# Performance work log

Hardware: AMD Instinct MI355X
Metric: run time of the kernel (lower is better)

Reference implementation:

```python
import jax, jax.numpy as jnp
import numpy as np

K = 6  # number of deformation subdivision steps
LEVEL = 5  # icosphere subdivision level -> 10242 verts, 20480 faces
EPS = 1e-12


def _icosphere(level):
    t = (1.0 + 5.0 ** 0.5) / 2.0
    verts = np.array([
        [-1, t, 0], [1, t, 0], [-1, -t, 0], [1, -t, 0],
        [0, -1, t], [0, 1, t], [0, -1, -t], [0, 1, -t],
        [t, 0, -1], [t, 0, 1], [-t, 0, -1], [-t, 0, 1]], dtype=np.float64)
    verts /= np.linalg.norm(verts, axis=1, keepdims=True)
    faces = [[0, 11, 5], [0, 5, 1], [0, 1, 7], [0, 7, 10], [0, 10, 11],
             [1, 5, 9], [5, 11, 4], [11, 10, 2], [10, 7, 6], [7, 1, 8],
             [3, 9, 4], [3, 4, 2], [3, 2, 6], [3, 6, 8], [3, 8, 9],
             [4, 9, 5], [2, 4, 11], [6, 2, 10], [8, 6, 7], [9, 8, 1]]
    for _ in range(level):
        vlist = [v for v in verts]
        cache = {}
        def mid(a, b):
            key = (min(a, b), max(a, b))
            if key not in cache:
                m = vlist[a] + vlist[b]
                m = m / np.linalg.norm(m)
                vlist.append(m)
                cache[key] = len(vlist) - 1
            return cache[key]
        new_faces = []
        for a, b, c in faces:
            ab, bc, ca = mid(a, b), mid(b, c), mid(c, a)
            new_faces += [[a, ab, ca], [b, bc, ab], [c, ca, bc], [ab, bc, ca]]
        faces = new_faces
        verts = np.stack(vlist)
    return verts.astype(np.float32), np.asarray(faces, dtype=np.int32)


def _norm(a):
    return a / jnp.maximum(jnp.linalg.norm(a, axis=-1, keepdims=True), EPS)


def setup_inputs() -> dict:
    key = jax.random.key(0)
    v_np, f_np = _icosphere(LEVEL)  # [10242,3], [20480,3]
    x = jax.random.normal(key, (v_np.shape[0], 6), dtype=jnp.float32)
    return {"x": x, "v": jnp.asarray(v_np), "f": jnp.asarray(f_np)}


def _forward(x, v, f):
    # Build rotation frame from the 6D feature
    rot_x = _norm(x[..., :3])
    rot_z = _norm(jnp.cross(rot_x, x[..., 3:]))
    rot_y = _norm(jnp.cross(rot_z, rot_x))
    # Axis-angle of the rotation matrix with rows (rot_x, rot_y, rot_z)
    axis = jnp.concatenate([
        rot_y[..., 2:3] - rot_z[..., 1:2],
        rot_z[..., 0:1] - rot_x[..., 2:3],
        rot_x[..., 1:2] - rot_y[..., 0:1]], axis=-1)
    trace = (rot_x[..., 0:1] + rot_y[..., 1:2] + rot_z[..., 2:3] - 1.0) * 0.5
    trace = jnp.clip(trace, -1.0 + 1e-7, 1.0 - 1e-7)
    angle = -jnp.arccos(trace) / (2 ** K)
    axis = _norm(axis)
    # Rodrigues rotation of mesh vertices by angle/2^k about per-point axis
    dot = jnp.sum(axis * v, axis=-1, keepdims=True)
    cross = jnp.cross(axis, v)
    cos, sin = jnp.cos(angle), jnp.sin(angle)
    p = v * cos + cross * sin + axis * (dot * (1.0 - cos))  # [N,3]
    # Nearest-triangle search data: face centers on the sphere
    centers = _norm(v[f].mean(axis=1))  # [F,3]
    for _ in range(K):
        p = _norm(p)
        # Nearest face by center direction; [N,F] score matrix (memory-bound)
        fid = jnp.argmax(p @ centers.T, axis=-1)  # [N]
        tri = v[f[fid]]  # [N,3,3] gathered triangle vertices
        # Gnomonic barycentric coords: solve [v0 v1 v2] b = p, normalize
        b = jnp.linalg.solve(jnp.swapaxes(tri, -1, -2), p[..., None])[..., 0]
        bary = b / jnp.sum(b, axis=-1, keepdims=True)  # [N,3]
        # Barycentric gather-interpolate of current point field
        p = jnp.sum(p[f[fid]] * bary[..., None], axis=-2)  # [N,3]
    return _norm(p)


def reference(x, v, f):
    return _forward(x, v, f)
```

## Files before the change

kernel.cpp:

```cpp
#include <hip/hip_runtime.h>
#include <hip/hip_bf16.h>
#include <math.h>

#define EPSN 1e-12f
#define MARGIN 0.02f
#define NBLK 256
#define NTHR 1024

typedef unsigned long long u64;
union F4U { float4 f; u64 u[2]; };

__device__ __forceinline__ float4 cload(const float4* p)
{
    F4U r;
    const u64* q = (const u64*)p;
    r.u[0] = __hip_atomic_load(q + 0, __ATOMIC_RELAXED, __HIP_MEMORY_SCOPE_AGENT);
    r.u[1] = __hip_atomic_load(q + 1, __ATOMIC_RELAXED, __HIP_MEMORY_SCOPE_AGENT);
    return r.f;
}

__device__ __forceinline__ void cstore(float4* p, float4 v)
{
    F4U s; s.f = v;
    u64* q = (u64*)p;
    __hip_atomic_store(q + 0, s.u[0], __ATOMIC_RELAXED, __HIP_MEMORY_SCOPE_AGENT);
    __hip_atomic_store(q + 1, s.u[1], __ATOMIC_RELAXED, __HIP_MEMORY_SCOPE_AGENT);
}

__device__ __forceinline__ int cload_i(const int* p)
{
    return __hip_atomic_load(p, __ATOMIC_RELAXED, __HIP_MEMORY_SCOPE_AGENT);
}

__device__ __forceinline__ void cstore_i(int* p, int v)
{
    __hip_atomic_store(p, v, __ATOMIC_RELAXED, __HIP_MEMORY_SCOPE_AGENT);
}

__global__ __launch_bounds__(1024)
void zero_kernel(int* __restrict__ flags)
{
    for (int i = threadIdx.x; i < 8192; i += 1024) flags[i] = 0;
}

__device__ __forceinline__ void grid_barrier(int* __restrict__ arrive,
                                             int* __restrict__ release,
                                             int target)
{
    asm volatile("s_waitcnt vmcnt(0)" ::: "memory");
    __syncthreads();
    if (threadIdx.x == 0)
        cstore_i(&arrive[blockIdx.x * 16], target);
    if (blockIdx.x == 0 && threadIdx.x < 64) {
        const int l = threadIdx.x;
        for (;;) {
            int a0 = cload_i(&arrive[l * 16]);
            int a1 = cload_i(&arrive[(l + 64) * 16]);
            int a2 = cload_i(&arrive[(l + 128) * 16]);
            int a3 = cload_i(&arrive[(l + 192) * 16]);
            if (__all(min(min(a0, a1), min(a2, a3)) >= target)) break;
            __builtin_amdgcn_s_sleep(2);
        }
        if (l == 0) cstore_i(release, target);
    }
    if (threadIdx.x == 0) {
        while (cload_i(release) < target)
            __builtin_amdgcn_s_sleep(2);
    }
    __syncthreads();
}

__global__ __launch_bounds__(NTHR)
void persist_kernel(const float* __restrict__ x,
                    const float* __restrict__ v,
                    const int* __restrict__ f,
                    float4* __restrict__ fine4,
                    float4* __restrict__ coarse4,
                    float4* __restrict__ v4,
                    float4* __restrict__ pA,
                    float4* __restrict__ pB,
                    float* __restrict__ out,
                    int* __restrict__ arrive,
                    int* __restrict__ release,
                    int N, int F)
{
    const int tid  = threadIdx.x;
    const int lane = tid & 63;
    const int t    = blockIdx.x * NTHR + tid;
    const int gw   = t >> 6;
    const int NW   = (NBLK * NTHR) >> 6;
    const int C    = F >> 6;

    if (gw < C) {
        int fi = (gw << 6) + lane;
        int a = f[fi * 3 + 0], b = f[fi * 3 + 1], c = f[fi * 3 + 2];
        float mx = v[a * 3 + 0] + v[b * 3 + 0] + v[c * 3 + 0];
        float my = v[a * 3 + 1] + v[b * 3 + 1] + v[c * 3 + 1];
        float mz = v[a * 3 + 2] + v[b * 3 + 2] + v[c * 3 + 2];
        float r = 1.0f / fmaxf(sqrtf(mx * mx + my * my + mz * mz), EPSN);
        float fx = mx * r, fy = my * r, fz = mz * r;
        cstore(&fine4[fi], make_float4(fx, fy, fz, 0.0f));
        float sx = fx, sy = fy, sz = fz;
        for (int off = 32; off >= 1; off >>= 1) {
            sx += __shfl_xor(sx, off);
            sy += __shfl_xor(sy, off);
            sz += __shfl_xor(sz, off);
        }
        if (lane == 0) {
            float rr = 1.0f / fmaxf(sqrtf(sx * sx + sy * sy + sz * sz), EPSN);
            cstore(&coarse4[gw], make_float4(sx * rr, sy * rr, sz * rr, 0.0f));
        }
    }

    if (t < N) {
        float ax = x[t * 6 + 0], ay = x[t * 6 + 1], az = x[t * 6 + 2];
        float bx = x[t * 6 + 3], by = x[t * 6 + 4], bz = x[t * 6 + 5];

        float l = fmaxf(sqrtf(ax * ax + ay * ay + az * az), EPSN);
        float rxx = ax / l, rxy = ay / l, rxz = az / l;
        float czx = rxy * bz - rxz * by;
        float czy = rxz * bx - rxx * bz;
        float czz = rxx * by - rxy * bx;
        l = fmaxf(sqrtf(czx * czx + czy * czy + czz * czz), EPSN);
        float rzx = czx / l, rzy = czy / l, rzz = czz / l;
        float cyx = rzy * rxz - rzz * rxy;
        float cyy = rzz * rxx - rzx * rxz;
        float cyz = rzx * rxy - rzy * rxx;
        l = fmaxf(sqrtf(cyx * cyx + cyy * cyy + cyz * cyz), EPSN);
        float ryx = cyx / l, ryy = cyy / l, ryz = cyz / l;

        float axx = ryz - rzy;
        float axy = rzx - rxz;
        float axz = rxy - ryx;
        float trace = (rxx + ryy + rzz - 1.0f) * 0.5f;
        trace = fminf(fmaxf(trace, -1.0f + 1e-7f), 1.0f - 1e-7f);
        float angle = -acosf(trace) * (1.0f / 64.0f);
        l = fmaxf(sqrtf(axx * axx + axy * axy + axz * axz), EPSN);
        axx /= l; axy /= l; axz /= l;

        float vx = v[t * 3 + 0], vy = v[t * 3 + 1], vz = v[t * 3 + 2];
        float d = axx * vx + axy * vy + axz * vz;
        float crx = axy * vz - axz * vy;
        float cry = axz * vx - axx * vz;
        float crz = axx * vy - axy * vx;
        float s, c;
        sincosf(angle, &s, &c);
        float omc = 1.0f - c;
        cstore(&pA[t], make_float4(vx * c + crx * s + axx * (d * omc),
                                   vy * c + cry * s + axy * (d * omc),
                                   vz * c + crz * s + axz * (d * omc), 0.0f));
        cstore(&v4[t], make_float4(vx, vy, vz, 0.0f));
    }

    grid_barrier(arrive, release, 1);

    float4 c0 = coarse4[lane];
    float4 c1 = coarse4[lane + 64];
    float4 c2 = coarse4[lane + 128];
    float4 c3 = coarse4[lane + 192];
    float4 c4 = coarse4[lane + 256];

    const float4* pin = pA;
    float4* pout = pB;

    #pragma unroll 1
    for (int k = 0; k < 6; ++k) {
        const bool last = (k == 5);
        for (int pt = gw; pt < N; pt += NW) {
            float4 p = cload(&pin[pt]);
            float rl = 1.0f / fmaxf(sqrtf(p.x * p.x + p.y * p.y + p.z * p.z), EPSN);
            float pnx = p.x * rl, pny = p.y * rl, pnz = p.z * rl;

            float s0 = pnx * c0.x + pny * c0.y + pnz * c0.z;
            float s1 = pnx * c1.x + pny * c1.y + pnz * c1.z;
            float s2 = pnx * c2.x + pny * c2.y + pnz * c2.z;
            float s3 = pnx * c3.x + pny * c3.y + pnz * c3.z;
            float s4 = pnx * c4.x + pny * c4.y + pnz * c4.z;

            float bs = fmaxf(fmaxf(fmaxf(s0, s1), fmaxf(s2, s3)), s4);
            for (int off = 32; off >= 1; off >>= 1)
                bs = fmaxf(bs, __shfl_xor(bs, off));
            const float thr = bs - MARGIN;

            float best = -1e30f;
            int bidx = 0;
            unsigned long long m;
            #define EXPAND(CC)                                                \
                {                                                             \
                    int cand = ((CC) << 6) + lane;                            \
                    float4 fc = fine4[cand];                                  \
                    float sc = pnx * fc.x + pny * fc.y + pnz * fc.z;          \
                    if (sc > best) { best = sc; bidx = cand; }                \
                }
            m = __ballot(s0 >= thr);
            while (m) { int src = __ffsll(m) - 1; m &= m - 1; EXPAND(src); }
            m = __ballot(s1 >= thr);
            while (m) { int src = __ffsll(m) - 1; m &= m - 1; EXPAND(src + 64); }
            m = __ballot(s2 >= thr);
            while (m) { int src = __ffsll(m) - 1; m &= m - 1; EXPAND(src + 128); }
            m = __ballot(s3 >= thr);
            while (m) { int src = __ffsll(m) - 1; m &= m - 1; EXPAND(src + 192); }
            m = __ballot(s4 >= thr);
            while (m) { int src = __ffsll(m) - 1; m &= m - 1; EXPAND(src + 256); }
            #undef EXPAND

            for (int off = 32; off >= 1; off >>= 1) {
                float sx2 = __shfl_xor(best, off);
                int   ix2 = __shfl_xor(bidx, off);
                if (sx2 > best || (sx2 == best && ix2 < bidx)) { best = sx2; bidx = ix2; }
            }

            if (lane == 0) {
                int i0 = f[bidx * 3 + 0];
                int i1 = f[bidx * 3 + 1];
                int i2 = f[bidx * 3 + 2];
                float4 A = v4[i0];
                float4 B = v4[i1];
                float4 Cv = v4[i2];
                float4 q0 = cload(&pin[i0]);
                float4 q1 = cload(&pin[i1]);
                float4 q2 = cload(&pin[i2]);

                float bcx = B.y * Cv.z - B.z * Cv.y;
                float bcy = B.z * Cv.x - B.x * Cv.z;
                float bcz = B.x * Cv.y - B.y * Cv.x;
                float D0 = pnx * bcx + pny * bcy + pnz * bcz;
                float pcx = pny * Cv.z - pnz * Cv.y;
                float pcy = pnz * Cv.x - pnx * Cv.z;
                float pcz = pnx * Cv.y - pny * Cv.x;
                float D1 = A.x * pcx + A.y * pcy + A.z * pcz;
                float bpx = B.y * pnz - B.z * pny;
                float bpy = B.z * pnx - B.x * pnz;
                float bpz = B.x * pny - B.y * pnx;
                float D2 = A.x * bpx + A.y * bpy + A.z * bpz;

                float inv = 1.0f / (D0 + D1 + D2);
                float w0 = D0 * inv, w1 = D1 * inv, w2 = D2 * inv;

                float r0 = 1.0f / fmaxf(sqrtf(q0.x * q0.x + q0.y * q0.y + q0.z * q0.z), EPSN);
                float r1 = 1.0f / fmaxf(sqrtf(q1.x * q1.x + q1.y * q1.y + q1.z * q1.z), EPSN);
                float r2 = 1.0f / fmaxf(sqrtf(q2.x * q2.x + q2.y * q2.y + q2.z * q2.z), EPSN);

                float ox = w0 * q0.x * r0 + w1 * q1.x * r1 + w2 * q2.x * r2;
                float oy = w0 * q0.y * r0 + w1 * q1.y * r1 + w2 * q2.y * r2;
                float oz = w0 * q0.z * r0 + w1 * q1.z * r1 + w2 * q2.z * r2;

                if (last) {
                    float r = 1.0f / fmaxf(sqrtf(ox * ox + oy * oy + oz * oz), EPSN);
                    out[pt * 3 + 0] = ox * r;
                    out[pt * 3 + 1] = oy * r;
                    out[pt * 3 + 2] = oz * r;
                } else {
                    cstore(&pout[pt], make_float4(ox, oy, oz, 0.0f));
                }
            }
        }
        if (!last) grid_barrier(arrive, release, k + 2);
        const float4* tp = pin; pin = pout; pout = (float4*)tp;
    }
}

extern "C" void kernel_launch(void* const* d_in, const int* in_sizes, int n_in,
                              void* d_out, int out_size, void* d_ws, size_t ws_size,
                              hipStream_t stream)
{
    const float* x = (const float*)d_in[0];
    const float* v = (const float*)d_in[1];
    const int*   f = (const int*)d_in[2];
    float* out = (float*)d_out;

    int N = in_sizes[1] / 3;
    int F = in_sizes[2] / 3;
    const int C = F >> 6;

    char* ws = (char*)d_ws;
    int* arrive  = (int*)ws;
    int* release = (int*)(ws + 16384);
    size_t off = 32768;
    float4* fine4   = (float4*)(ws + off); off += (size_t)F * sizeof(float4);
    float4* coarse4 = (float4*)(ws + off); off += (size_t)C * sizeof(float4);
    float4* v4      = (float4*)(ws + off); off += (size_t)N * sizeof(float4);
    float4* p0      = (float4*)(ws + off); off += (size_t)N * sizeof(float4);
    float4* p1      = (float4*)(ws + off);

    zero_kernel<<<1, 1024, 0, stream>>>(arrive);
    persist_kernel<<<NBLK, NTHR, 0, stream>>>(
        x, v, f, fine4, coarse4, v4, p0, p1, out, arrive, release, N, F);
}
```

Before: 155.1 us.

## Size persistent grid from occupancy query and prefetch next point per wave

The persistent kernel's block count is now picked at launch from the device CU count and the occupancy query, allowing two 1024-thread blocks per CU, with __launch_bounds__ raised to request that. The grid barrier now scans a variable number of arrival flags, and setup loops stride over points. The per-wave point loop loads the next point before working on the current one to hide load latency. More blocks give more waves per CU, at the cost of register pressure and a costlier barrier, and host property queries now run on every launch.

After: 173.2 us. +11.7%, slower.

```diff
diff --git a/kernel.cpp b/kernel.cpp
--- a/kernel.cpp
+++ b/kernel.cpp
@@ -4,7 +4,6 @@
 
 #define EPSN 1e-12f
 #define MARGIN 0.02f
-#define NBLK 256
 #define NTHR 1024
 
 typedef unsigned long long u64;
@@ -40,12 +39,12 @@
 __global__ __launch_bounds__(1024)
 void zero_kernel(int* __restrict__ flags)
 {
-    for (int i = threadIdx.x; i < 8192; i += 1024) flags[i] = 0;
+    for (int i = threadIdx.x; i < 12288; i += 1024) flags[i] = 0;
 }
 
 __device__ __forceinline__ void grid_barrier(int* __restrict__ arrive,
                                              int* __restrict__ release,
-                                             int target)
+                                             int target, int nblk)
 {
     asm volatile("s_waitcnt vmcnt(0)" ::: "memory");
     __syncthreads();
@@ -54,11 +53,10 @@
     if (blockIdx.x == 0 && threadIdx.x < 64) {
         const int l = threadIdx.x;
         for (;;) {
-            int a0 = cload_i(&arrive[l * 16]);
-            int a1 = cload_i(&arrive[(l + 64) * 16]);
-            int a2 = cload_i(&arrive[(l + 128) * 16]);
-            int a3 = cload_i(&arrive[(l + 192) * 16]);
-            if (__all(min(min(a0, a1), min(a2, a3)) >= target)) break;
+            int mn = 0x7fffffff;
+            for (int i = l; i < nblk; i += 64)
+                mn = min(mn, cload_i(&arrive[i * 16]));
+            if (__all(mn >= target)) break;
             __builtin_amdgcn_s_sleep(2);
         }
         if (l == 0) cstore_i(release, target);
@@ -70,7 +68,7 @@
     __syncthreads();
 }
 
-__global__ __launch_bounds__(NTHR)
+__global__ __launch_bounds__(NTHR, 8)
 void persist_kernel(const float* __restrict__ x,
                     const float* __restrict__ v,
                     const int* __restrict__ f,
@@ -82,13 +80,13 @@
                     float* __restrict__ out,
                     int* __restrict__ arrive,
                     int* __restrict__ release,
-                    int N, int F)
+                    int N, int F, int nblk)
 {
     const int tid  = threadIdx.x;
     const int lane = tid & 63;
     const int t    = blockIdx.x * NTHR + tid;
     const int gw   = t >> 6;
-    const int NW   = (NBLK * NTHR) >> 6;
+    const int NW   = (nblk * NTHR) >> 6;
     const int C    = F >> 6;
 
     if (gw < C) {
@@ -112,9 +110,9 @@
         }
     }
 
-    if (t < N) {
-        float ax = x[t * 6 + 0], ay = x[t * 6 + 1], az = x[t * 6 + 2];
-        float bx = x[t * 6 + 3], by = x[t * 6 + 4], bz = x[t * 6 + 5];
+    for (int n = t; n < N; n += nblk * NTHR) {
+        float ax = x[n * 6 + 0], ay = x[n * 6 + 1], az = x[n * 6 + 2];
+        float bx = x[n * 6 + 3], by = x[n * 6 + 4], bz = x[n * 6 + 5];
 
         float l = fmaxf(sqrtf(ax * ax + ay * ay + az * az), EPSN);
         float rxx = ax / l, rxy = ay / l, rxz = az / l;
@@ -138,7 +136,7 @@
         l = fmaxf(sqrtf(axx * axx + axy * axy + axz * axz), EPSN);
         axx /= l; axy /= l; axz /= l;
 
-        float vx = v[t * 3 + 0], vy = v[t * 3 + 1], vz = v[t * 3 + 2];
+        float vx = v[n * 3 + 0], vy = v[n * 3 + 1], vz = v[n * 3 + 2];
         float d = axx * vx + axy * vy + axz * vz;
         float crx = axy * vz - axz * vy;
         float cry = axz * vx - axx * vz;
@@ -146,13 +144,13 @@
         float s, c;
         sincosf(angle, &s, &c);
         float omc = 1.0f - c;
-        cstore(&pA[t], make_float4(vx * c + crx * s + axx * (d * omc),
+        cstore(&pA[n], make_float4(vx * c + crx * s + axx * (d * omc),
                                    vy * c + cry * s + axy * (d * omc),
                                    vz * c + crz * s + axz * (d * omc), 0.0f));
-        cstore(&v4[t], make_float4(vx, vy, vz, 0.0f));
-    }
-
-    grid_barrier(arrive, release, 1);
+        cstore(&v4[n], make_float4(vx, vy, vz, 0.0f));
+    }
+
+    grid_barrier(arrive, release, 1, nblk);
 
     float4 c0 = coarse4[lane];
     float4 c1 = coarse4[lane + 64];
@@ -166,10 +164,18 @@
     #pragma unroll 1
     for (int k = 0; k < 6; ++k) {
         const bool last = (k == 5);
-        for (int pt = gw; pt < N; pt += NW) {
-            float4 p = cload(&pin[pt]);
-            float rl = 1.0f / fmaxf(sqrtf(p.x * p.x + p.y * p.y + p.z * p.z), EPSN);
-            float pnx = p.x * rl, pny = p.y * rl, pnz = p.z * rl;
+        int pt = gw;
+        float4 pcur = make_float4(0.f, 0.f, 0.f, 0.f);
+        if (pt < N) pcur = cload(&pin[pt]);
+        #pragma unroll 1
+        while (pt < N) {
+            const int ptn = pt + NW;
+            float4 pnext = make_float4(0.f, 0.f, 0.f, 0.f);
+            if (ptn < N) pnext = cload(&pin[ptn]);
+
+            float rl = 1.0f / fmaxf(sqrtf(pcur.x * pcur.x + pcur.y * pcur.y +
+                                          pcur.z * pcur.z), EPSN);
+            float pnx = pcur.x * rl, pny = pcur.y * rl, pnz = pcur.z * rl;
 
             float s0 = pnx * c0.x + pny * c0.y + pnz * c0.z;
             float s1 = pnx * c1.x + pny * c1.y + pnz * c1.z;
@@ -254,8 +260,10 @@
                     cstore(&pout[pt], make_float4(ox, oy, oz, 0.0f));
                 }
             }
+            pt = ptn;
+            pcur = pnext;
         }
-        if (!last) grid_barrier(arrive, release, k + 2);
+        if (!last) grid_barrier(arrive, release, k + 2, nblk);
         const float4* tp = pin; pin = pout; pout = (float4*)tp;
     }
 }
@@ -275,15 +283,25 @@
 
     char* ws = (char*)d_ws;
     int* arrive  = (int*)ws;
-    int* release = (int*)(ws + 16384);
-    size_t off = 32768;
+    int* release = (int*)(ws + 32768);
+    size_t off = 36864;
     float4* fine4   = (float4*)(ws + off); off += (size_t)F * sizeof(float4);
     float4* coarse4 = (float4*)(ws + off); off += (size_t)C * sizeof(float4);
     float4* v4      = (float4*)(ws + off); off += (size_t)N * sizeof(float4);
     float4* p0      = (float4*)(ws + off); off += (size_t)N * sizeof(float4);
     float4* p1      = (float4*)(ws + off);
 
+    int perCU = 1;
+    if (hipOccupancyMaxActiveBlocksPerMultiprocessor(&perCU, persist_kernel,
+                                                     NTHR, 0) != hipSuccess)
+        perCU = 1;
+    int cus = 256;
+    hipDeviceProp_t prop;
+    if (hipGetDeviceProperties(&prop, 0) == hipSuccess && prop.multiProcessorCount > 0)
+        cus = prop.multiProcessorCount;
+    const int nblk = cus * (perCU >= 2 ? 2 : 1);
+
     zero_kernel<<<1, 1024, 0, stream>>>(arrive);
-    persist_kernel<<<NBLK, NTHR, 0, stream>>>(
-        x, v, f, fine4, coarse4, v4, p0, p1, out, arrive, release, N, F);
-}
+    persist_kernel<<<nblk, NTHR, 0, stream>>>(
+        x, v, f, fine4, coarse4, v4, p0, p1, out, arrive, release, N, F, nblk);
+}
```
